# Kernel tuning notes

Hardware: AMD Instinct MI355X
Metric: run time of the kernel (lower is better)

Reference implementation:

```python
import jax, jax.numpy as jnp
from jax import lax
import numpy as np

DIVISOR = 2.0  # init kwarg 'divisor'


def setup_inputs() -> dict:
    key = jax.random.key(0)
    k1, k2, k3, k4 = jax.random.split(key, 4)
    x = jax.random.normal(k1, (8, 32, 32, 64, 64), dtype=jnp.float32)        # N,C_in,D,H,W
    conv_weight = jax.random.normal(k2, (64, 32, 3, 3, 3), dtype=jnp.float32)  # O,I,kD,kH,kW
    conv_bias = jax.random.normal(k3, (64,), dtype=jnp.float32)
    bias = jax.random.normal(k4, (64, 1, 1, 1), dtype=jnp.float32)           # post bias (per out-channel)
    return {"x": x, "conv_weight": conv_weight, "conv_bias": conv_bias, "bias": bias}


def reference(x, conv_weight, conv_bias, bias):
    # Valid 3D conv, stride 1 (matches the CUDA kernel's sliding window)
    y = lax.conv_general_dilated(
        x, conv_weight,
        window_strides=(1, 1, 1), padding='VALID',
        dimension_numbers=('NCDHW', 'OIDHW', 'NCDHW'))
    # (conv + conv_bias) / divisor + post_bias, then sum over out-channels
    y = (y + conv_bias[None, :, None, None, None]) * (1.0 / DIVISOR) \
        + bias.reshape(1, -1, 1, 1, 1)
    return jnp.sum(y, axis=1)  # (N, D_out, H_out, W_out)
```

## Files before the change

kernel.cpp:

```cpp
#include <hip/hip_runtime.h>


#define XD 32
#define XH 64
#define XW 64
#define DOUT 30
#define HOUT 62
#define WOUT 62
#define DT 4
#define HT 8
#define TILE_SLICES 6
#define TILE_ROWS 10
#define TILE_FLOATS (TILE_SLICES * TILE_ROWS * 64)
#define CHUNKS (TILE_FLOATS / 4)
#define CH_STRIDE (XD * XH * XW)

__global__ __launch_bounds__(256, 2)
void conv3d_chansum_kernel(const float* __restrict__ x,
                           const float* __restrict__ cw,
                           const float* __restrict__ cb,
                           const float* __restrict__ pb,
                           float* __restrict__ out) {
  __shared__ float tile[2][TILE_FLOATS];
  __shared__ float wl[897];

  const int tid = threadIdx.x;
  const int hb = blockIdx.x;
  const int db = blockIdx.y;
  const int n  = blockIdx.z;
  const int h0 = hb * HT;
  const int d0 = db * DT;

  const int s    = tid & 7;
  const int slot = tid >> 3;
  const int dt   = slot >> 3;
  const int ht   = slot & 7;

  const float* xn = x + (size_t)n * (32u * CH_STRIDE);

  int  soff[4];
  bool svalid[4];
#pragma unroll
  for (int round = 0; round < 4; ++round) {
    int k   = tid + round * 256;
    int sd  = k / 160;
    int rem = k - sd * 160;
    int r   = rem >> 4;
    int c   = rem & 15;
    int csrc = c ^ ((sd * 10 + r) & 15);
    int dd = d0 + sd, hh = h0 + r;
    svalid[round] = (k < CHUNKS) & (dd < XD) & (hh < XH);
    soff[round]   = dd * (XH * XW) + hh * XW + csrc * 4;
  }
  const int ldsoff = (tid & ~63) * 4;

  auto stage = [&](float* buf, int ch) {
    const float* xnc = xn + (size_t)ch * CH_STRIDE;
#pragma unroll
    for (int round = 0; round < 4; ++round) {
      if (svalid[round]) {
        __builtin_amdgcn_global_load_lds(
            (const __attribute__((address_space(1))) void*)(xnc + soff[round]),
            (__attribute__((address_space(3))) void*)(buf + round * 1024 + ldsoff),
            16, 0, 0);
      }
    }
  };

  float acc[8];
#pragma unroll
  for (int j = 0; j < 8; ++j) acc[j] = 0.f;

  stage(tile[0], 0);
  for (int e = tid; e < 864; e += 256) {
    int i = e / 27;
    int j = e - i * 27;
    float ssum = 0.f;
#pragma unroll 8
    for (int o = 0; o < 64; ++o) ssum += cw[o * 864 + e];
    wl[i * 28 + j] = 0.5f * ssum;
  }
  if (tid == 0) {
    float ssum = 0.f;
    for (int o = 0; o < 64; ++o) ssum += 0.5f * cb[o] + pb[o];
    wl[896] = ssum;
  }
  __syncthreads();

#pragma unroll 1
  for (int ch = 0; ch < 32; ++ch) {
    const float* buf = tile[ch & 1];
    if (ch < 31) stage(tile[(ch & 1) ^ 1], ch + 1);

    float wr[28];
#pragma unroll
    for (int q = 0; q < 7; ++q)
      *(float4*)&wr[4 * q] = *(const float4*)&wl[ch * 28 + 4 * q];

#pragma unroll
    for (int kd = 0; kd < 3; ++kd) {
#pragma unroll
      for (int kh = 0; kh < 3; ++kh) {
        const int row  = (dt + kd) * TILE_ROWS + (ht + kh);
        const int key  = row & 15;
        const int base = row * 64;
        float4 a  = *(const float4*)&buf[base + (((2 * s) ^ key) << 2)];
        float4 b  = *(const float4*)&buf[base + (((2 * s + 1) ^ key) << 2)];
        float2 c2 = *(const float2*)&buf[base + ((((2 * s + 2) & 15) ^ key) << 2)];
        float xv[10] = {a.x, a.y, a.z, a.w, b.x, b.y, b.z, b.w, c2.x, c2.y};
        const int wb = kd * 9 + kh * 3;
#pragma unroll
        for (int j = 0; j < 8; ++j)
          acc[j] = fmaf(xv[j], wr[wb],
                   fmaf(xv[j + 1], wr[wb + 1],
                   fmaf(xv[j + 2], wr[wb + 2], acc[j])));
      }
    }

    __syncthreads();
  }

  const float Cc  = wl[896];
  const int   dow = d0 + dt, how = h0 + ht;
  if (dow < DOUT && how < HOUT) {
    float* op = out + (((size_t)n * DOUT + dow) * HOUT + how) * WOUT + s * 8;
    const int nw = min(8, WOUT - s * 8);
#pragma unroll
    for (int j = 0; j < 4; ++j) {
      if (2 * j < nw) {
        float2 v;
        v.x = acc[2 * j] + Cc;
        v.y = acc[2 * j + 1] + Cc;
        *(float2*)&op[2 * j] = v;
      }
    }
  }
}

extern "C" void kernel_launch(void* const* d_in, const int* in_sizes, int n_in,
                              void* d_out, int out_size, void* d_ws, size_t ws_size,
                              hipStream_t stream) {
  const float* x  = (const float*)d_in[0];
  const float* cw = (const float*)d_in[1];
  const float* cb = (const float*)d_in[2];
  const float* pb = (const float*)d_in[3];
  float* out = (float*)d_out;

  dim3 grid(8, 8, 8);
  conv3d_chansum_kernel<<<grid, 256, 0, stream>>>(x, cw, cb, pb, out);
}
```

Measured before the change: 236.4 us.

## Compute two output depth slices per thread to reuse LDS rows

Halves the block to 128 threads. Each thread now accumulates two depth outputs, so every loaded input row feeds up to two accumulators across kd, which cuts LDS reads per FMA. The XOR swizzle is replaced by a fixed permutation of 16-byte chunks, so each thread's read offsets are constant. The cost is fewer threads per block, doubled accumulator registers, and twice as many staging load rounds per thread.

```diff
diff --git a/kernel.cpp b/kernel.cpp
--- a/kernel.cpp
+++ b/kernel.cpp
@@ -13,9 +13,10 @@
 #define TILE_ROWS 10
 #define TILE_FLOATS (TILE_SLICES * TILE_ROWS * 64)
 #define CHUNKS (TILE_FLOATS / 4)
+#define ROUNDS 8
 #define CH_STRIDE (XD * XH * XW)
 
-__global__ __launch_bounds__(256, 2)
+__global__ __launch_bounds__(128, 2)
 void conv3d_chansum_kernel(const float* __restrict__ x,
                            const float* __restrict__ cw,
                            const float* __restrict__ cb,
@@ -33,21 +34,22 @@
 
   const int s    = tid & 7;
   const int slot = tid >> 3;
-  const int dt   = slot >> 3;
   const int ht   = slot & 7;
+  const int dts  = slot >> 3;
 
   const float* xn = x + (size_t)n * (32u * CH_STRIDE);
 
-  int  soff[4];
-  bool svalid[4];
+  int  soff[ROUNDS];
+  bool svalid[ROUNDS];
 #pragma unroll
-  for (int round = 0; round < 4; ++round) {
-    int k   = tid + round * 256;
+  for (int round = 0; round < ROUNDS; ++round) {
+    int k   = tid + round * 128;
     int sd  = k / 160;
     int rem = k - sd * 160;
     int r   = rem >> 4;
-    int c   = rem & 15;
-    int csrc = c ^ ((sd * 10 + r) & 15);
+    int p   = rem & 15;
+    int t1  = (11 * p) & 15;
+    int csrc = (t1 < 8) ? (2 * t1) : (2 * ((11 * (p - 8)) & 15) + 1);
     int dd = d0 + sd, hh = h0 + r;
     svalid[round] = (k < CHUNKS) & (dd < XD) & (hh < XH);
     soff[round]   = dd * (XH * XW) + hh * XW + csrc * 4;
@@ -57,22 +59,28 @@
   auto stage = [&](float* buf, int ch) {
     const float* xnc = xn + (size_t)ch * CH_STRIDE;
 #pragma unroll
-    for (int round = 0; round < 4; ++round) {
+    for (int round = 0; round < ROUNDS; ++round) {
       if (svalid[round]) {
         __builtin_amdgcn_global_load_lds(
             (const __attribute__((address_space(1))) void*)(xnc + soff[round]),
-            (__attribute__((address_space(3))) void*)(buf + round * 1024 + ldsoff),
+            (__attribute__((address_space(3))) void*)(buf + round * 512 + ldsoff),
             16, 0, 0);
       }
     }
   };
 
-  float acc[8];
+  const int P0 = (3 * s) & 15;
+  const int P1 = (3 * s + 8) & 15;
+  const int P2 = (3 * s + 3) & 15;
+
+  float acc[2][8];
 #pragma unroll
-  for (int j = 0; j < 8; ++j) acc[j] = 0.f;
+  for (int dl = 0; dl < 2; ++dl)
+#pragma unroll
+    for (int j = 0; j < 8; ++j) acc[dl][j] = 0.f;
 
   stage(tile[0], 0);
-  for (int e = tid; e < 864; e += 256) {
+  for (int e = tid; e < 864; e += 128) {
     int i = e / 27;
     int j = e - i * 27;
     float ssum = 0.f;
@@ -98,22 +106,27 @@
       *(float4*)&wr[4 * q] = *(const float4*)&wl[ch * 28 + 4 * q];
 
 #pragma unroll
-    for (int kd = 0; kd < 3; ++kd) {
+    for (int i = 0; i < 4; ++i) {
+      const int slice = 2 * dts + i;
 #pragma unroll
       for (int kh = 0; kh < 3; ++kh) {
-        const int row  = (dt + kd) * TILE_ROWS + (ht + kh);
-        const int key  = row & 15;
-        const int base = row * 64;
-        float4 a  = *(const float4*)&buf[base + (((2 * s) ^ key) << 2)];
-        float4 b  = *(const float4*)&buf[base + (((2 * s + 1) ^ key) << 2)];
-        float2 c2 = *(const float2*)&buf[base + ((((2 * s + 2) & 15) ^ key) << 2)];
+        const int base = (slice * TILE_ROWS + (ht + kh)) * 64;
+        float4 a  = *(const float4*)&buf[base + (P0 << 2)];
+        float4 b  = *(const float4*)&buf[base + (P1 << 2)];
+        float2 c2 = *(const float2*)&buf[base + (P2 << 2)];
         float xv[10] = {a.x, a.y, a.z, a.w, b.x, b.y, b.z, b.w, c2.x, c2.y};
-        const int wb = kd * 9 + kh * 3;
 #pragma unroll
-        for (int j = 0; j < 8; ++j)
-          acc[j] = fmaf(xv[j], wr[wb],
-                   fmaf(xv[j + 1], wr[wb + 1],
-                   fmaf(xv[j + 2], wr[wb + 2], acc[j])));
+        for (int kd = 0; kd < 3; ++kd) {
+          const int dl = i - kd;
+          if (dl >= 0 && dl < 2) {
+            const int wb = kd * 9 + kh * 3;
+#pragma unroll
+            for (int j = 0; j < 8; ++j)
+              acc[dl][j] = fmaf(xv[j], wr[wb],
+                           fmaf(xv[j + 1], wr[wb + 1],
+                           fmaf(xv[j + 2], wr[wb + 2], acc[dl][j])));
+          }
+        }
       }
     }
 
@@ -121,17 +134,21 @@
   }
 
   const float Cc  = wl[896];
-  const int   dow = d0 + dt, how = h0 + ht;
-  if (dow < DOUT && how < HOUT) {
-    float* op = out + (((size_t)n * DOUT + dow) * HOUT + how) * WOUT + s * 8;
-    const int nw = min(8, WOUT - s * 8);
+  const int   how = h0 + ht;
+  const int   nw  = min(8, WOUT - s * 8);
 #pragma unroll
-    for (int j = 0; j < 4; ++j) {
-      if (2 * j < nw) {
-        float2 v;
-        v.x = acc[2 * j] + Cc;
-        v.y = acc[2 * j + 1] + Cc;
-        *(float2*)&op[2 * j] = v;
+  for (int dl = 0; dl < 2; ++dl) {
+    const int dow = d0 + 2 * dts + dl;
+    if (dow < DOUT && how < HOUT) {
+      float* op = out + (((size_t)n * DOUT + dow) * HOUT + how) * WOUT + s * 8;
+#pragma unroll
+      for (int j = 0; j < 4; ++j) {
+        if (2 * j < nw) {
+          float2 v;
+          v.x = acc[dl][2 * j] + Cc;
+          v.y = acc[dl][2 * j + 1] + Cc;
+          *(float2*)&op[2 * j] = v;
+        }
       }
     }
   }
@@ -147,5 +164,5 @@
   float* out = (float*)d_out;
 
   dim3 grid(8, 8, 8);
-  conv3d_chansum_kernel<<<grid, 256, 0, stream>>>(x, cw, cb, pb, out);
+  conv3d_chansum_kernel<<<grid, 128, 0, stream>>>(x, cw, cb, pb, out);
 }
```

New measurement: 249.2 us. +5.4%, slower.

## Give each wave private double-buffered tiles and drop block-wide barriers

Applied to the files above, without the earlier changes.

Each wavefront now stages its own 3-slice input tile into a per-wave LDS double buffer and waits on its own loads with vmcnt and lgkmcnt, instead of the whole block sharing one tile and calling __syncthreads every channel. The LDS swizzle is changed so each lane reads two float4s, and the two extra input values come from the neighbouring lane through a DPP move rather than a third LDS read. This removes block-wide barrier stalls and some LDS traffic. In exchange, halo slices are loaded redundantly across waves, LDS usage grows, and correctness depends on the lane-to-lane DPP pattern and the hand-written waitcnt counts.

```diff
diff --git a/kernel.cpp b/kernel.cpp
--- a/kernel.cpp
+++ b/kernel.cpp
@@ -7,13 +7,13 @@
 #define DOUT 30
 #define HOUT 62
 #define WOUT 62
-#define DT 4
-#define HT 8
-#define TILE_SLICES 6
-#define TILE_ROWS 10
-#define TILE_FLOATS (TILE_SLICES * TILE_ROWS * 64)
-#define CHUNKS (TILE_FLOATS / 4)
 #define CH_STRIDE (XD * XH * XW)
+#define WBUF_FLOATS 2048
+
+__device__ __forceinline__ float nextlane(float v) {
+  return __int_as_float(
+      __builtin_amdgcn_mov_dpp(__float_as_int(v), 0x101, 0xF, 0xF, true));
+}
 
 __global__ __launch_bounds__(256, 2)
 void conv3d_chansum_kernel(const float* __restrict__ x,
@@ -21,57 +21,47 @@
                            const float* __restrict__ cb,
                            const float* __restrict__ pb,
                            float* __restrict__ out) {
-  __shared__ float tile[2][TILE_FLOATS];
+  __shared__ float wavebuf[4][2][WBUF_FLOATS];
   __shared__ float wl[897];
 
-  const int tid = threadIdx.x;
-  const int hb = blockIdx.x;
-  const int db = blockIdx.y;
-  const int n  = blockIdx.z;
-  const int h0 = hb * HT;
-  const int d0 = db * DT;
-
-  const int s    = tid & 7;
-  const int slot = tid >> 3;
-  const int dt   = slot >> 3;
-  const int ht   = slot & 7;
+  const int tid  = threadIdx.x;
+  const int wid  = tid >> 6;
+  const int lane = tid & 63;
+  const int hb = blockIdx.x, db = blockIdx.y, n = blockIdx.z;
+  const int h0 = hb * 8, d0 = db * 4;
+  const int s  = tid & 7;
+  const int ht = (tid >> 3) & 7;
+  const bool alive = (d0 + wid) < DOUT;
 
   const float* xn = x + (size_t)n * (32u * CH_STRIDE);
 
-  int  soff[4];
-  bool svalid[4];
+  int soff[8];
 #pragma unroll
-  for (int round = 0; round < 4; ++round) {
-    int k   = tid + round * 256;
+  for (int i = 0; i < 8; ++i) {
+    int k   = 64 * i + lane;
     int sd  = k / 160;
     int rem = k - sd * 160;
-    int r   = rem >> 4;
-    int c   = rem & 15;
-    int csrc = c ^ ((sd * 10 + r) & 15);
-    int dd = d0 + sd, hh = h0 + r;
-    svalid[round] = (k < CHUNKS) & (dd < XD) & (hh < XH);
-    soff[round]   = dd * (XH * XW) + hh * XW + csrc * 4;
+    int rr  = rem >> 4;
+    int p   = rem & 15;
+    int t1  = (11 * p) & 15;
+    int csrc = (t1 < 8) ? (2 * t1) : (2 * ((11 * (p - 8)) & 15) + 1);
+    int dd = min(d0 + wid + sd, XD - 1);
+    int hh = min(h0 + rr, XH - 1);
+    soff[i] = dd * (XH * XW) + hh * XW + csrc * 4;
   }
-  const int ldsoff = (tid & ~63) * 4;
 
   auto stage = [&](float* buf, int ch) {
     const float* xnc = xn + (size_t)ch * CH_STRIDE;
 #pragma unroll
-    for (int round = 0; round < 4; ++round) {
-      if (svalid[round]) {
-        __builtin_amdgcn_global_load_lds(
-            (const __attribute__((address_space(1))) void*)(xnc + soff[round]),
-            (__attribute__((address_space(3))) void*)(buf + round * 1024 + ldsoff),
-            16, 0, 0);
-      }
+    for (int i = 0; i < 8; ++i) {
+      __builtin_amdgcn_global_load_lds(
+          (const __attribute__((address_space(1))) void*)(xnc + soff[i]),
+          (__attribute__((address_space(3))) void*)(buf + i * 256),
+          16, 0, 0);
     }
   };
 
-  float acc[8];
-#pragma unroll
-  for (int j = 0; j < 8; ++j) acc[j] = 0.f;
-
-  stage(tile[0], 0);
+  if (alive) stage(&wavebuf[wid][0][0], 0);
   for (int e = tid; e < 864; e += 256) {
     int i = e / 27;
     int j = e - i * 27;
@@ -86,12 +76,23 @@
     wl[896] = ssum;
   }
   __syncthreads();
+  if (!alive) return;
+
+  const int P0 = (3 * s) & 15;
+  const int P1 = (3 * s + 8) & 15;
+
+  float acc[8];
+#pragma unroll
+  for (int j = 0; j < 8; ++j) acc[j] = 0.f;
 
 #pragma unroll 1
   for (int ch = 0; ch < 32; ++ch) {
-    const float* buf = tile[ch & 1];
-    if (ch < 31) stage(tile[(ch & 1) ^ 1], ch + 1);
+    const int chn = (ch < 31) ? ch + 1 : 31;
+    stage(&wavebuf[wid][(ch + 1) & 1][0], chn);
+    asm volatile("s_waitcnt vmcnt(8)" ::: "memory");
+    __builtin_amdgcn_sched_barrier(0);
 
+    const float* buf = &wavebuf[wid][ch & 1][0];
     float wr[28];
 #pragma unroll
     for (int q = 0; q < 7; ++q)
@@ -101,13 +102,12 @@
     for (int kd = 0; kd < 3; ++kd) {
 #pragma unroll
       for (int kh = 0; kh < 3; ++kh) {
-        const int row  = (dt + kd) * TILE_ROWS + (ht + kh);
-        const int key  = row & 15;
-        const int base = row * 64;
-        float4 a  = *(const float4*)&buf[base + (((2 * s) ^ key) << 2)];
-        float4 b  = *(const float4*)&buf[base + (((2 * s + 1) ^ key) << 2)];
-        float2 c2 = *(const float2*)&buf[base + ((((2 * s + 2) & 15) ^ key) << 2)];
-        float xv[10] = {a.x, a.y, a.z, a.w, b.x, b.y, b.z, b.w, c2.x, c2.y};
+        const int base = (kd * 10 + ht + kh) * 64;
+        float4 a = *(const float4*)&buf[base + (P0 << 2)];
+        float4 b = *(const float4*)&buf[base + (P1 << 2)];
+        float x8 = nextlane(a.x);
+        float x9 = nextlane(a.y);
+        float xv[10] = {a.x, a.y, a.z, a.w, b.x, b.y, b.z, b.w, x8, x9};
         const int wb = kd * 9 + kh * 3;
 #pragma unroll
         for (int j = 0; j < 8; ++j)
@@ -117,12 +117,13 @@
       }
     }
 
-    __syncthreads();
+    asm volatile("s_waitcnt lgkmcnt(0)" ::: "memory");
+    __builtin_amdgcn_sched_barrier(0);
   }
 
   const float Cc  = wl[896];
-  const int   dow = d0 + dt, how = h0 + ht;
-  if (dow < DOUT && how < HOUT) {
+  const int   dow = d0 + wid, how = h0 + ht;
+  if (how < HOUT) {
     float* op = out + (((size_t)n * DOUT + dow) * HOUT + how) * WOUT + s * 8;
     const int nw = min(8, WOUT - s * 8);
 #pragma unroll
```

Result: faster. 224.6 us (-5.0%).
